# Kernel optimization log

Hardware: AMD Instinct MI355X
Metric: run time of the kernel (lower is better)

The kernel has to match this reference:

```python
import jax, jax.numpy as jnp
import numpy as np

N_NODES = 50000
N_EDGES = 800000
HEADS = 5
NFEAT = 5
C1 = 32  # hidden_layers


def setup_inputs() -> dict:
    key = jax.random.key(0)
    ks = jax.random.split(key, 20)
    s = 0.3  # glorot-ish scale
    d = {
        "x": jax.random.normal(ks[0], (N_NODES, NFEAT), jnp.float32),
        "edge_attr": jax.random.uniform(ks[1], (N_EDGES, 1), jnp.float32),
        "src": jax.random.randint(ks[2], (N_EDGES,), 0, N_NODES, jnp.int32),
        "dst": jax.random.randint(ks[3], (N_EDGES,), 0, N_NODES, jnp.int32),
        # conv1: in=5 -> heads=5, out=32, concat
        "W1": jax.random.normal(ks[4], (NFEAT, HEADS * C1), jnp.float32) * s,
        "a_src1": jax.random.normal(ks[5], (HEADS, C1), jnp.float32) * s,
        "a_dst1": jax.random.normal(ks[6], (HEADS, C1), jnp.float32) * s,
        "We1": jax.random.normal(ks[7], (1, HEADS * C1), jnp.float32) * s,
        "ae1": jax.random.normal(ks[8], (HEADS, C1), jnp.float32) * s,
        "b1": jnp.zeros((HEADS * C1,), jnp.float32),
        # conv2: in=160 -> heads=5, out=1, mean over heads
        "W2": jax.random.normal(ks[9], (HEADS * C1, HEADS * 1), jnp.float32) * 0.08,
        "a_src2": jax.random.normal(ks[10], (HEADS, 1), jnp.float32) * s,
        "a_dst2": jax.random.normal(ks[11], (HEADS, 1), jnp.float32) * s,
        "We2": jax.random.normal(ks[12], (1, HEADS * 1), jnp.float32) * s,
        "ae2": jax.random.normal(ks[13], (HEADS, 1), jnp.float32) * s,
        "b2": jnp.zeros((1,), jnp.float32),
        "Wlin": jax.random.normal(ks[14], (1, 1), jnp.float32),
    }
    return d


def gat_layer(x, src, dst, eattr, W, a_src, a_dst, We, a_e, bias, concat, n_nodes):
    """PyG GATConv with edge_dim, self-loops already added by caller."""
    H, C = a_src.shape
    h = (x @ W).reshape(-1, H, C)                      # [N,H,C]
    alpha_s = (h * a_src[None]).sum(-1)                # [N,H]
    alpha_d = (h * a_dst[None]).sum(-1)                # [N,H]
    ee = (eattr @ We).reshape(-1, H, C)                # [E,H,C]
    alpha_e = (ee * a_e[None]).sum(-1)                 # [E,H]
    logits = jax.nn.leaky_relu(alpha_s[src] + alpha_d[dst] + alpha_e, 0.2)
    # segment softmax over destination nodes
    m = jax.ops.segment_max(logits, dst, num_segments=n_nodes)
    m = jnp.where(jnp.isfinite(m), m, 0.0)
    ex = jnp.exp(logits - m[dst])
    denom = jax.ops.segment_sum(ex, dst, num_segments=n_nodes)
    alpha = ex / (denom[dst] + 1e-16)                  # [E,H]
    msg = (alpha[:, :, None] * h[src]).reshape(-1, H * C)
    agg = jax.ops.segment_sum(msg, dst, num_segments=n_nodes).reshape(n_nodes, H, C)
    if concat:
        return agg.reshape(n_nodes, H * C) + bias
    return agg.mean(axis=1) + bias


def reference(x, edge_attr, src, dst, W1, a_src1, a_dst1, We1, ae1, b1,
              W2, a_src2, a_dst2, We2, ae2, b2, Wlin):
    n = x.shape[0]
    loop = jnp.arange(n, dtype=src.dtype)
    s = jnp.concatenate([src, loop])
    t = jnp.concatenate([dst, loop])
    # self-loop edge_attr = mean of edge_attr (PyG fill_value='mean')
    ea_loop = jnp.broadcast_to(edge_attr.mean(axis=0, keepdims=True), (n, edge_attr.shape[1]))
    ea = jnp.concatenate([edge_attr, ea_loop], axis=0)

    x1 = gat_layer(x, s, t, ea, W1, a_src1, a_dst1, We1, ae1, b1, True, n)
    x2 = jax.nn.relu(x1)
    # dropout p=0.2 is identity in eval mode
    x4 = gat_layer(x2, s, t, ea, W2, a_src2, a_dst2, We2, ae2, b2, False, n)
    x5 = x4 @ Wlin                                     # Linear(1,1,bias=False)
    return jax.nn.sigmoid(x5)                          # [N,1]
```

## Files before the change

kernel.cpp:

```cpp
#include <hip/hip_runtime.h>
#include <hip/hip_fp16.h>
#include <math.h>

#define N_NODES 50000
#define N_EDGES 800000
#define E2 (N_EDGES + N_NODES)
#define HEADS 5
#define C1 32
#define F1 160

#define BSZ 64
#define NBK 782
#define NBL 128
#define CH  6641
#define MTOT (NBK*NBL)
#define MC  391
#define GRID_H1 (N_NODES/4)
#define CAP 1408

static constexpr size_t alignup(size_t x){ return (x + 255) & ~size_t(255); }
static constexpr size_t OFF_SCAL  = 0;
static constexpr size_t OFF_H     = alignup(OFF_SCAL + 64*4);
static constexpr size_t OFF_EAS   = alignup(OFF_H    + (size_t)MTOT*4);
static constexpr size_t OFF_PART  = alignup(OFF_EAS  + (size_t)NBL*4);
static constexpr size_t OFF_PPREF = alignup(OFF_PART + (size_t)MC*4);
static constexpr size_t OFF_BST   = alignup(OFF_PPREF+ (size_t)MC*4);
static constexpr size_t OFF_OFFS  = alignup(OFF_BST  + (size_t)(NBK+1)*4);
static constexpr size_t OFF_BPACK = alignup(OFF_OFFS + (size_t)(N_NODES+1)*4);
static constexpr size_t OFF_EDG   = alignup(OFF_BPACK+ (size_t)E2*8);
static constexpr size_t OFF_AS1P  = alignup(OFF_EDG  + (size_t)E2*4);
static constexpr size_t OFF_AD1P  = alignup(OFF_AS1P + (size_t)N_NODES*8*4);
static constexpr size_t OFF_IDEN1 = alignup(OFF_AD1P + (size_t)N_NODES*8*4);
static constexpr size_t OFF_G16   = alignup(OFF_IDEN1+ (size_t)N_NODES*8*4);
static constexpr size_t OFF_AD2P  = alignup(OFF_G16  + (size_t)N_NODES*16*2);
static constexpr size_t OFF_H1Q   = alignup(OFF_AD2P + (size_t)N_NODES*8*4);
static constexpr size_t OFF_X2H   = alignup(OFF_H1Q  + (size_t)N_NODES*F1);
static constexpr size_t OFF_ALPH  = alignup(OFF_X2H  + (size_t)N_NODES*F1*2);

typedef float vf2 __attribute__((ext_vector_type(2)));
__device__ __forceinline__ float2 fp8x2_to_f32(unsigned short r){
  vf2 v = __builtin_amdgcn_cvt_pk_f32_fp8((int)r, false);
  return make_float2(v.x, v.y);
}
__device__ __forceinline__ float4 fp8x4_to_f32(unsigned int r){
  vf2 lo = __builtin_amdgcn_cvt_pk_f32_fp8((int)r, false);
  vf2 hi = __builtin_amdgcn_cvt_pk_f32_fp8((int)r, true);
  return make_float4(lo.x, lo.y, hi.x, hi.y);
}

__global__ __launch_bounds__(320) void k_init(const float* __restrict__ x, const float* __restrict__ W1,
                       const float* __restrict__ as1w, const float* __restrict__ ad1w,
                       unsigned short* __restrict__ h1q, float* __restrict__ as1p, float* __restrict__ ad1p,
                       const int* __restrict__ dst, const float* __restrict__ ea,
                       int* __restrict__ H, float* __restrict__ easum){
  __shared__ float sW[5*F1];
  int t = threadIdx.x;
  if (blockIdx.x < GRID_H1){
    for (int k = t; k < 5*F1; k += 320) sW[k] = W1[k];
    __syncthreads();
    int nl = t / 80;
    int c  = t - nl*80;
    int n  = blockIdx.x*4 + nl;
    int c0 = 2*c;
    float hv0 = 0.f, hv1 = 0.f;
    #pragma unroll
    for (int f = 0; f < 5; f++){
      float xv = x[n*5 + f];
      hv0 += xv * sW[f*F1 + c0];
      hv1 += xv * sW[f*F1 + c0 + 1];
    }
    int pk = __builtin_amdgcn_cvt_pk_fp8_f32(hv0, hv1, 0, false);
    h1q[n*80 + c] = (unsigned short)(pk & 0xFFFF);
    float vs = hv0*as1w[c0] + hv1*as1w[c0+1];
    float vd = hv0*ad1w[c0] + hv1*ad1w[c0+1];
    #pragma unroll
    for (int m = 8; m >= 1; m >>= 1){
      vs += __shfl_xor(vs, m, 64);
      vd += __shfl_xor(vd, m, 64);
    }
    if ((c & 15) == 0){
      int h = c >> 4;
      as1p[n*8 + h] = vs;
      ad1p[n*8 + h] = vd;
    }
  } else {
    int* hist = (int*)sW;
    float* wsum = (float*)&hist[NBK + 1];
    for (int k = t; k < NBK; k += 320) hist[k] = 0;
    __syncthreads();
    int b = blockIdx.x - GRID_H1;
    int e0 = b*CH, e1 = min(e0 + CH, E2);
    float s = 0.f;
    for (int e = e0 + t; e < e1; e += 320){
      int d;
      if (e < N_EDGES){ d = dst[e]; s += ea[e]; }
      else d = e - N_EDGES;
      atomicAdd(&hist[d >> 6], 1);
    }
    #pragma unroll
    for (int m = 1; m < 64; m <<= 1) s += __shfl_xor(s, m, 64);
    if ((t & 63) == 0) wsum[t >> 6] = s;
    __syncthreads();
    for (int k = t; k < NBK; k += 320) H[(size_t)k*NBL + b] = hist[k];
    if (t == 0) easum[b] = wsum[0] + wsum[1] + wsum[2] + wsum[3] + wsum[4];
  }
}

__global__ void k_s1(const int* __restrict__ H, int* __restrict__ partial){
  int i = blockIdx.x*256 + threadIdx.x;
  int v = (i < MTOT) ? H[i] : 0;
  #pragma unroll
  for (int m = 1; m < 64; m <<= 1) v += __shfl_xor(v, m, 64);
  __shared__ int sh[4];
  if ((threadIdx.x & 63) == 0) sh[threadIdx.x >> 6] = v;
  __syncthreads();
  if (threadIdx.x == 0) partial[blockIdx.x] = sh[0] + sh[1] + sh[2] + sh[3];
}

__global__ __launch_bounds__(512) void k_s2p(const int* __restrict__ partial, int* __restrict__ ppref,
                      int* __restrict__ offs, int* __restrict__ bstart,
                      const float* __restrict__ easum,
                      const float* __restrict__ We1, const float* __restrict__ ae1,
                      const float* __restrict__ We2, const float* __restrict__ ae2,
                      float* __restrict__ scal){
  __shared__ int sp[512];
  __shared__ float sh_ea[NBL];
  int t = threadIdx.x;
  if (t < NBL) sh_ea[t] = easum[t];
  if (t >= 448 && t < 448 + HEADS){
    int h = t - 448;
    float s = 0.f;
    for (int c = 0; c < C1; c++) s += We1[h*C1 + c] * ae1[h*C1 + c];
    scal[2 + h] = s;
    scal[7 + h] = We2[h] * ae2[h];
  }
  int v = (t < MC) ? partial[t] : 0;
  sp[t] = v;
  __syncthreads();
  if (t == 511){
    float es = 0.f;
    for (int i = 0; i < NBL; i++) es += sh_ea[i];
    scal[1] = es / (float)N_EDGES;
  }
  for (int off = 1; off < 512; off <<= 1){
    int u = (t >= off) ? sp[t - off] : 0;
    __syncthreads();
    sp[t] += u;
    __syncthreads();
  }
  if (t < MC) ppref[t] = sp[t] - v;
  if (t == 0){ offs[N_NODES] = E2; bstart[NBK] = E2; }
}

__global__ void k_s3(int* __restrict__ H, const int* __restrict__ ppref, int* __restrict__ bstart){
  __shared__ int sp[256];
  int b = blockIdx.x, t = threadIdx.x;
  int i = b*256 + t;
  int v = (i < MTOT) ? H[i] : 0;
  sp[t] = v;
  __syncthreads();
  for (int off = 1; off < 256; off <<= 1){
    int u = (t >= off) ? sp[t - off] : 0;
    __syncthreads();
    sp[t] += u;
    __syncthreads();
  }
  int P = ppref[b] + sp[t] - v;
  if (i < MTOT){
    H[i] = P;
    if (i % NBL == 0) bstart[i / NBL] = P;
  }
}

__global__ __launch_bounds__(256) void k_scat(const int* __restrict__ src, const int* __restrict__ dst,
                       const float* __restrict__ ea, const float* __restrict__ scal,
                       const int* __restrict__ H, int2* __restrict__ bpack){
  __shared__ int lofs[NBK];
  int b = blockIdx.x;
  for (int k = threadIdx.x; k < NBK; k += 256) lofs[k] = H[(size_t)k*NBL + b];
  __syncthreads();
  float mean = scal[1];
  int e0 = b*CH, e1 = min(e0 + CH, E2);
  for (int e = e0 + threadIdx.x; e < e1; e += 256){
    int d, s; float a;
    if (e < N_EDGES){ d = dst[e]; s = src[e]; a = ea[e]; }
    else { d = s = e - N_EDGES; a = mean; }
    int pos = atomicAdd(&lofs[d >> 6], 1);
    bpack[pos] = make_int2(s | ((d & 63) << 16), __float_as_int(a));
  }
}

__global__ __launch_bounds__(256) void k_final2(const int* __restrict__ bstart,
                        const int2* __restrict__ bpack,
                        const float* __restrict__ as1p, const float* __restrict__ ad1p,
                        const float* __restrict__ scal,
                        int* __restrict__ offs, unsigned int* __restrict__ edge2,
                        __half* __restrict__ alpha, float* __restrict__ iden1){
  __shared__ int   cnt[BSZ], cur[BSZ];
  __shared__ float denL[BSZ*HEADS];
  __shared__ float adL [BSZ*HEADS];
  __shared__ unsigned int s_edge[CAP];
  __shared__ __half s_al[HEADS][CAP];
  int k = blockIdx.x, t = threadIdx.x;
  int base = k*BSZ;
  if (t < BSZ) cnt[t] = 0;
  for (int i = t; i < BSZ*HEADS; i += 256){
    int node = base + i/HEADS;
    adL[i] = (node < N_NODES) ? ad1p[node*8 + i%HEADS] : 0.f;
    denL[i] = 0.f;
  }
  __syncthreads();
  int r0 = bstart[k], r1 = bstart[k + 1];
  int sz = r1 - r0;
  for (int j = r0 + t; j < r1; j += 256) atomicAdd(&cnt[(bpack[j].x >> 16) & 63], 1);
  __syncthreads();
  if (t == 0){
    int run = 0;
    for (int i = 0; i < BSZ; i++){ int c = cnt[i]; cnt[i] = run; cur[i] = run; run += c; }
  }
  __syncthreads();
  if (t < BSZ){
    int n = base + t;
    if (n < N_NODES) offs[n] = r0 + cnt[t];
  }
  float wd[HEADS];
  #pragma unroll
  for (int h = 0; h < HEADS; h++) wd[h] = scal[2 + h];

  if (sz <= CAP){
    for (int j = r0 + t; j < r1; j += 256){
      int2 v = bpack[j];
      int s = v.x & 0xFFFF, loc = (v.x >> 16) & 63;
      float ea = __int_as_float(v.y);
      int lp = atomicAdd(&cur[loc], 1);
      s_edge[lp] = (unsigned int)s |
                   ((unsigned int)__half_as_ushort(__float2half(ea)) << 16);
      float4 g4 = *(const float4*)(as1p + s*8);
      float g5 = as1p[s*8 + 4];
      float g[HEADS] = {g4.x, g4.y, g4.z, g4.w, g5};
      #pragma unroll
      for (int h = 0; h < HEADS; h++){
        float lg = g[h] + adL[loc*HEADS + h] + ea*wd[h];
        lg = fmaxf(lg, 0.2f*lg);
        lg = fminf(lg, 10.f);
        float p = __expf(lg);
        s_al[h][lp] = __float2half(p);
        atomicAdd(&denL[loc*HEADS + h], p);
      }
    }
    __syncthreads();
    for (int i = t; i < sz; i += 256) edge2[r0 + i] = s_edge[i];
    #pragma unroll
    for (int h = 0; h < HEADS; h++)
      for (int i = t; i < sz; i += 256)
        alpha[(size_t)h*E2 + r0 + i] = s_al[h][i];
  } else {
    for (int j = r0 + t; j < r1; j += 256){
      int2 v = bpack[j];
      int s = v.x & 0xFFFF, loc = (v.x >> 16) & 63;
      float ea = __int_as_float(v.y);
      int pos = r0 + atomicAdd(&cur[loc], 1);
      edge2[pos] = (unsigned int)s |
                   ((unsigned int)__half_as_ushort(__float2half(ea)) << 16);
      float4 g4 = *(const float4*)(as1p + s*8);
      float g5 = as1p[s*8 + 4];
      float g[HEADS] = {g4.x, g4.y, g4.z, g4.w, g5};
      #pragma unroll
      for (int h = 0; h < HEADS; h++){
        float lg = g[h] + adL[loc*HEADS + h] + ea*wd[h];
        lg = fmaxf(lg, 0.2f*lg);
        lg = fminf(lg, 10.f);
        float p = __expf(lg);
        alpha[(size_t)h*E2 + pos] = __float2half(p);
        atomicAdd(&denL[loc*HEADS + h], p);
      }
    }
    __syncthreads();
  }
  for (int i = t; i < BSZ*HEADS; i += 256){
    int node = base + i/HEADS;
    if (node < N_NODES) iden1[node*8 + i%HEADS] = 1.f/(denL[i] + 1e-16f);
  }
}

__global__ __launch_bounds__(320) void k_agg1(const int* __restrict__ offs,
                      const unsigned int* __restrict__ edge2,
                      const __half* __restrict__ alpha, const float* __restrict__ iden1,
                      const unsigned short* __restrict__ h1q,
                      const float* __restrict__ b1, __half* __restrict__ x2h){
  int nl = threadIdx.x / 40;
  int c4 = threadIdx.x - nl*40;
  int n  = blockIdx.x*8 + nl;
  int h  = c4 >> 3;
  const __half* aph = alpha + (size_t)h*E2;
  const unsigned int* h1row = (const unsigned int*)h1q;
  int j0 = offs[n], j1 = offs[n + 1];
  float a0 = 0.f, a1 = 0.f, a2 = 0.f, a3 = 0.f;
  int j = j0;
  int jal = min(j1, (j0 + 3) & ~3);
  for (; j < jal; ++j){
    int s = edge2[j] & 0xFFFF;
    float a = __half2float(aph[j]);
    float4 f = fp8x4_to_f32(h1row[(size_t)s*40 + c4]);
    a0 += a*f.x; a1 += a*f.y; a2 += a*f.z; a3 += a*f.w;
  }
  for (; j + 7 < j1; j += 8){
    uint4  sa = *(const uint4*)(edge2 + j);
    uint4  sb = *(const uint4*)(edge2 + j + 4);
    union { uint2 u; __half2 h[2]; } UA; UA.u = *(const uint2*)(aph + j);
    union { uint2 u; __half2 h[2]; } UB; UB.u = *(const uint2*)(aph + j + 4);
    float2 A01 = __half22float2(UA.h[0]);
    float2 A23 = __half22float2(UA.h[1]);
    float2 A45 = __half22float2(UB.h[0]);
    float2 A67 = __half22float2(UB.h[1]);
    unsigned int r0 = h1row[(size_t)(sa.x & 0xFFFF)*40 + c4];
    unsigned int r1 = h1row[(size_t)(sa.y & 0xFFFF)*40 + c4];
    unsigned int r2 = h1row[(size_t)(sa.z & 0xFFFF)*40 + c4];
    unsigned int r3 = h1row[(size_t)(sa.w & 0xFFFF)*40 + c4];
    unsigned int r4 = h1row[(size_t)(sb.x & 0xFFFF)*40 + c4];
    unsigned int r5 = h1row[(size_t)(sb.y & 0xFFFF)*40 + c4];
    unsigned int r6 = h1row[(size_t)(sb.z & 0xFFFF)*40 + c4];
    unsigned int r7 = h1row[(size_t)(sb.w & 0xFFFF)*40 + c4];
    float4 f0 = fp8x4_to_f32(r0), f1 = fp8x4_to_f32(r1);
    float4 f2 = fp8x4_to_f32(r2), f3 = fp8x4_to_f32(r3);
    float4 f4 = fp8x4_to_f32(r4), f5 = fp8x4_to_f32(r5);
    float4 f6 = fp8x4_to_f32(r6), f7 = fp8x4_to_f32(r7);
    a0 += A01.x*f0.x; a1 += A01.x*f0.y; a2 += A01.x*f0.z; a3 += A01.x*f0.w;
    a0 += A01.y*f1.x; a1 += A01.y*f1.y; a2 += A01.y*f1.z; a3 += A01.y*f1.w;
    a0 += A23.x*f2.x; a1 += A23.x*f2.y; a2 += A23.x*f2.z; a3 += A23.x*f2.w;
    a0 += A23.y*f3.x; a1 += A23.y*f3.y; a2 += A23.y*f3.z; a3 += A23.y*f3.w;
    a0 += A45.x*f4.x; a1 += A45.x*f4.y; a2 += A45.x*f4.z; a3 += A45.x*f4.w;
    a0 += A45.y*f5.x; a1 += A45.y*f5.y; a2 += A45.y*f5.z; a3 += A45.y*f5.w;
    a0 += A67.x*f6.x; a1 += A67.x*f6.y; a2 += A67.x*f6.z; a3 += A67.x*f6.w;
    a0 += A67.y*f7.x; a1 += A67.y*f7.y; a2 += A67.y*f7.z; a3 += A67.y*f7.w;
  }
  for (; j + 3 < j1; j += 4){
    uint4  ss = *(const uint4*)(edge2 + j);
    union { uint2 u; __half2 h[2]; } UA; UA.u = *(const uint2*)(aph + j);
    float2 A01 = __half22float2(UA.h[0]);
    float2 A23 = __half22float2(UA.h[1]);
    float4 f0 = fp8x4_to_f32(h1row[(size_t)(ss.x & 0xFFFF)*40 + c4]);
    float4 f1 = fp8x4_to_f32(h1row[(size_t)(ss.y & 0xFFFF)*40 + c4]);
    float4 f2 = fp8x4_to_f32(h1row[(size_t)(ss.z & 0xFFFF)*40 + c4]);
    float4 f3 = fp8x4_to_f32(h1row[(size_t)(ss.w & 0xFFFF)*40 + c4]);
    a0 += A01.x*f0.x; a1 += A01.x*f0.y; a2 += A01.x*f0.z; a3 += A01.x*f0.w;
    a0 += A01.y*f1.x; a1 += A01.y*f1.y; a2 += A01.y*f1.z; a3 += A01.y*f1.w;
    a0 += A23.x*f2.x; a1 += A23.x*f2.y; a2 += A23.x*f2.z; a3 += A23.x*f2.w;
    a0 += A23.y*f3.x; a1 += A23.y*f3.y; a2 += A23.y*f3.z; a3 += A23.y*f3.w;
  }
  for (; j < j1; ++j){
    int s = edge2[j] & 0xFFFF;
    float a = __half2float(aph[j]);
    float4 f = fp8x4_to_f32(h1row[(size_t)s*40 + c4]);
    a0 += a*f.x; a1 += a*f.y; a2 += a*f.z; a3 += a*f.w;
  }
  float inv = iden1[n*8 + h];
  float4 bb = *(const float4*)(b1 + 4*c4);
  float v0 = fmaxf(a0*inv + bb.x, 0.f);
  float v1 = fmaxf(a1*inv + bb.y, 0.f);
  float v2 = fmaxf(a2*inv + bb.z, 0.f);
  float v3 = fmaxf(a3*inv + bb.w, 0.f);
  __half2 o0 = __floats2half2_rn(v0, v1);
  __half2 o1 = __floats2half2_rn(v2, v3);
  *(uint2*)(x2h + (size_t)n*F1 + 4*c4) =
      make_uint2(*(unsigned int*)&o0, *(unsigned int*)&o1);
}

__global__ __launch_bounds__(256) void k_h2(const __half* __restrict__ x2h, const float* __restrict__ W2,
                    const float* __restrict__ asw2, const float* __restrict__ adw2,
                    __half* __restrict__ G16, float* __restrict__ ad2p){
  __shared__ float sW[F1*HEADS];
  for (int k = threadIdx.x; k < F1*HEADS; k += 256) sW[k] = W2[k];
  __syncthreads();
  int w = threadIdx.x >> 6, l = threadIdx.x & 63;
  int n = blockIdx.x*4 + w;
  const __half2* x22 = (const __half2*)x2h;
  float acc[HEADS] = {0.f, 0.f, 0.f, 0.f, 0.f};
  for (int k2 = l; k2 < 80; k2 += 64){
    float2 f = __half22float2(x22[(size_t)n*80 + k2]);
    #pragma unroll
    for (int h = 0; h < HEADS; h++)
      acc[h] += f.x * sW[(2*k2)*HEADS + h] + f.y * sW[(2*k2+1)*HEADS + h];
  }
  #pragma unroll
  for (int m = 1; m < 64; m <<= 1){
    #pragma unroll
    for (int h = 0; h < HEADS; h++) acc[h] += __shfl_xor(acc[h], m, 64);
  }
  if (l == 0){
    #pragma unroll
    for (int h = 0; h < HEADS; h++){
      G16[(size_t)n*16 + h]     = __float2half(acc[h]);
      G16[(size_t)n*16 + 5 + h] = __float2half(acc[h] * asw2[h]);
      ad2p[n*8 + h]             = acc[h] * adw2[h];
    }
    #pragma unroll
    for (int z = 10; z < 16; z++) G16[(size_t)n*16 + z] = __float2half(0.f);
  }
}

__global__ __launch_bounds__(256) void k_agg2(const int* __restrict__ offs,
                      const unsigned int* __restrict__ edge2,
                      const __half* __restrict__ G16, const float* __restrict__ ad2p,
                      const float* __restrict__ scal,
                      const float* __restrict__ b2, const float* __restrict__ Wlin,
                      float* __restrict__ out){
  int grp = threadIdx.x >> 4;
  int l16 = threadIdx.x & 15;
  int n = blockIdx.x*16 + grp;
  float adn[HEADS], wd[HEADS];
  #pragma unroll
  for (int h = 0; h < HEADS; h++){ adn[h] = ad2p[n*8 + h]; wd[h] = scal[7 + h]; }
  int j0 = offs[n], j1 = offs[n + 1];

  float den[HEADS] = {0,0,0,0,0};
  float ac[HEADS]  = {0,0,0,0,0};
  for (int j = j0 + l16; j < j1; j += 16){
    unsigned int e = edge2[j];
    int s = e & 0xFFFF;
    float c = __half2float(__ushort_as_half((unsigned short)(e >> 16)));
    const __half* gs = G16 + (size_t)s*16;
    union { uint4 u; __half2 h[4]; } U; U.u = *(const uint4*)gs;
    union { uint2 u; __half2 h[2]; } V; V.u = *(const uint2*)(gs + 8);
    float2 p01 = __half22float2(U.h[0]);
    float2 p23 = __half22float2(U.h[1]);
    float2 p45 = __half22float2(U.h[2]);
    float2 p67 = __half22float2(U.h[3]);
    float2 p89 = __half22float2(V.h[0]);
    float hv[HEADS] = {p01.x, p01.y, p23.x, p23.y, p45.x};
    float av[HEADS] = {p45.y, p67.x, p67.y, p89.x, p89.y};
    #pragma unroll
    for (int h = 0; h < HEADS; h++){
      float lg = av[h] + adn[h] + c*wd[h];
      lg = fmaxf(lg, 0.2f*lg);
      lg = fminf(lg, 50.f);
      float p = __expf(lg);
      den[h] += p;
      ac[h]  += p * hv[h];
    }
  }
  #pragma unroll
  for (int m = 1; m < 16; m <<= 1){
    #pragma unroll
    for (int h = 0; h < HEADS; h++){
      den[h] += __shfl_xor(den[h], m, 16);
      ac[h]  += __shfl_xor(ac[h], m, 16);
    }
  }
  if (l16 == 0){
    float v = 0.f;
    #pragma unroll
    for (int h = 0; h < HEADS; h++) v += ac[h] / (den[h] + 1e-16f);
    v = v * (1.f/HEADS) + b2[0];
    v *= Wlin[0];
    out[n] = 1.f / (1.f + __expf(-v));
  }
}

extern "C" void kernel_launch(void* const* d_in, const int* in_sizes, int n_in,
                              void* d_out, int out_size, void* d_ws, size_t ws_size,
                              hipStream_t stream) {
  const float* x    = (const float*)d_in[0];
  const float* ea   = (const float*)d_in[1];
  const int*   src  = (const int*)d_in[2];
  const int*   dst  = (const int*)d_in[3];
  const float* W1   = (const float*)d_in[4];
  const float* as1w = (const float*)d_in[5];
  const float* ad1w = (const float*)d_in[6];
  const float* We1  = (const float*)d_in[7];
  const float* ae1  = (const float*)d_in[8];
  const float* b1   = (const float*)d_in[9];
  const float* W2   = (const float*)d_in[10];
  const float* as2w = (const float*)d_in[11];
  const float* ad2w = (const float*)d_in[12];
  const float* We2  = (const float*)d_in[13];
  const float* ae2  = (const float*)d_in[14];
  const float* b2   = (const float*)d_in[15];
  const float* Wlin = (const float*)d_in[16];

  char* ws = (char*)d_ws;
  float* scal   = (float*)(ws + OFF_SCAL);
  int*   H      = (int*)  (ws + OFF_H);
  float* easum  = (float*)(ws + OFF_EAS);
  int*   part   = (int*)  (ws + OFF_PART);
  int*   ppref  = (int*)  (ws + OFF_PPREF);
  int*   bstart = (int*)  (ws + OFF_BST);
  int*   offs   = (int*)  (ws + OFF_OFFS);
  int2*  bpack  = (int2*) (ws + OFF_BPACK);
  unsigned int* edge2 = (unsigned int*)(ws + OFF_EDG);
  float* as1p   = (float*)(ws + OFF_AS1P);
  float* ad1p   = (float*)(ws + OFF_AD1P);
  float* iden1  = (float*)(ws + OFF_IDEN1);
  __half* G16   = (__half*)(ws + OFF_G16);
  float* ad2p   = (float*)(ws + OFF_AD2P);
  unsigned short* h1q = (unsigned short*)(ws + OFF_H1Q);
  __half* x2h   = (__half*)(ws + OFF_X2H);
  __half* alpha = (__half*)(ws + OFF_ALPH);
  float* outp   = (float*)d_out;

  k_init   <<<GRID_H1 + NBL, 320, 0, stream>>>(x, W1, as1w, ad1w, h1q, as1p, ad1p,
                                               dst, ea, H, easum);
  k_s1     <<<MC, 256, 0, stream>>>(H, part);
  k_s2p    <<<1, 512, 0, stream>>>(part, ppref, offs, bstart, easum, We1, ae1, We2, ae2, scal);
  k_s3     <<<MC, 256, 0, stream>>>(H, ppref, bstart);
  k_scat   <<<NBL, 256, 0, stream>>>(src, dst, ea, scal, H, bpack);
  k_final2 <<<NBK, 256, 0, stream>>>(bstart, bpack, as1p, ad1p, scal, offs, edge2, alpha, iden1);

  k_agg1   <<<N_NODES/8, 320, 0, stream>>>(offs, edge2, alpha, iden1, h1q, b1, x2h);
  k_h2     <<<N_NODES/4, 256, 0, stream>>>(x2h, W2, as2w, ad2w, G16, ad2p);
  k_agg2   <<<N_NODES/16, 256, 0, stream>>>(offs, edge2, G16, ad2p, scal, b2, Wlin, outp);
}
```

Before: 248.9 us.

## Fuse layer-1 attention logits and softmax denominator into aggregation kernel

Layer-1 edge attention weights and per-node softmax denominators are no longer computed in the CSR-building kernel and stored as a half-precision alpha array plus inverse-denominator array. The aggregation kernel now computes the logits, exponentials and denominator on the fly from as1p, ad1p and the packed edge attribute. This removes about 8.5 MB of alpha writes and reads, the shared-memory atomics for the denominator, and one intermediate buffer. In exchange the exp work is repeated by each of the 8 lanes sharing a head, extra gathers of as1p are added, and the 4-wide and alignment loops are dropped.

```diff
diff --git a/kernel.cpp b/kernel.cpp
--- a/kernel.cpp
+++ b/kernel.cpp
@@ -30,18 +30,12 @@
 static constexpr size_t OFF_EDG   = alignup(OFF_BPACK+ (size_t)E2*8);
 static constexpr size_t OFF_AS1P  = alignup(OFF_EDG  + (size_t)E2*4);
 static constexpr size_t OFF_AD1P  = alignup(OFF_AS1P + (size_t)N_NODES*8*4);
-static constexpr size_t OFF_IDEN1 = alignup(OFF_AD1P + (size_t)N_NODES*8*4);
-static constexpr size_t OFF_G16   = alignup(OFF_IDEN1+ (size_t)N_NODES*8*4);
+static constexpr size_t OFF_G16   = alignup(OFF_AD1P + (size_t)N_NODES*8*4);
 static constexpr size_t OFF_AD2P  = alignup(OFF_G16  + (size_t)N_NODES*16*2);
 static constexpr size_t OFF_H1Q   = alignup(OFF_AD2P + (size_t)N_NODES*8*4);
 static constexpr size_t OFF_X2H   = alignup(OFF_H1Q  + (size_t)N_NODES*F1);
-static constexpr size_t OFF_ALPH  = alignup(OFF_X2H  + (size_t)N_NODES*F1*2);
 
 typedef float vf2 __attribute__((ext_vector_type(2)));
-__device__ __forceinline__ float2 fp8x2_to_f32(unsigned short r){
-  vf2 v = __builtin_amdgcn_cvt_pk_f32_fp8((int)r, false);
-  return make_float2(v.x, v.y);
-}
 __device__ __forceinline__ float4 fp8x4_to_f32(unsigned int r){
   vf2 lo = __builtin_amdgcn_cvt_pk_f32_fp8((int)r, false);
   vf2 hi = __builtin_amdgcn_cvt_pk_f32_fp8((int)r, true);
@@ -192,23 +186,12 @@
 
 __global__ __launch_bounds__(256) void k_final2(const int* __restrict__ bstart,
                         const int2* __restrict__ bpack,
-                        const float* __restrict__ as1p, const float* __restrict__ ad1p,
-                        const float* __restrict__ scal,
-                        int* __restrict__ offs, unsigned int* __restrict__ edge2,
-                        __half* __restrict__ alpha, float* __restrict__ iden1){
-  __shared__ int   cnt[BSZ], cur[BSZ];
-  __shared__ float denL[BSZ*HEADS];
-  __shared__ float adL [BSZ*HEADS];
+                        int* __restrict__ offs, unsigned int* __restrict__ edge2){
+  __shared__ int cnt[BSZ], cur[BSZ];
   __shared__ unsigned int s_edge[CAP];
-  __shared__ __half s_al[HEADS][CAP];
   int k = blockIdx.x, t = threadIdx.x;
   int base = k*BSZ;
   if (t < BSZ) cnt[t] = 0;
-  for (int i = t; i < BSZ*HEADS; i += 256){
-    int node = base + i/HEADS;
-    adL[i] = (node < N_NODES) ? ad1p[node*8 + i%HEADS] : 0.f;
-    denL[i] = 0.f;
-  }
   __syncthreads();
   int r0 = bstart[k], r1 = bstart[k + 1];
   int sz = r1 - r0;
@@ -223,138 +206,105 @@
     int n = base + t;
     if (n < N_NODES) offs[n] = r0 + cnt[t];
   }
-  float wd[HEADS];
-  #pragma unroll
-  for (int h = 0; h < HEADS; h++) wd[h] = scal[2 + h];
-
   if (sz <= CAP){
     for (int j = r0 + t; j < r1; j += 256){
       int2 v = bpack[j];
-      int s = v.x & 0xFFFF, loc = (v.x >> 16) & 63;
-      float ea = __int_as_float(v.y);
-      int lp = atomicAdd(&cur[loc], 1);
-      s_edge[lp] = (unsigned int)s |
-                   ((unsigned int)__half_as_ushort(__float2half(ea)) << 16);
-      float4 g4 = *(const float4*)(as1p + s*8);
-      float g5 = as1p[s*8 + 4];
-      float g[HEADS] = {g4.x, g4.y, g4.z, g4.w, g5};
-      #pragma unroll
-      for (int h = 0; h < HEADS; h++){
-        float lg = g[h] + adL[loc*HEADS + h] + ea*wd[h];
-        lg = fmaxf(lg, 0.2f*lg);
-        lg = fminf(lg, 10.f);
-        float p = __expf(lg);
-        s_al[h][lp] = __float2half(p);
-        atomicAdd(&denL[loc*HEADS + h], p);
-      }
+      int lp = atomicAdd(&cur[(v.x >> 16) & 63], 1);
+      s_edge[lp] = (unsigned int)(v.x & 0xFFFF) |
+                   ((unsigned int)__half_as_ushort(__float2half(__int_as_float(v.y))) << 16);
     }
     __syncthreads();
     for (int i = t; i < sz; i += 256) edge2[r0 + i] = s_edge[i];
-    #pragma unroll
-    for (int h = 0; h < HEADS; h++)
-      for (int i = t; i < sz; i += 256)
-        alpha[(size_t)h*E2 + r0 + i] = s_al[h][i];
   } else {
     for (int j = r0 + t; j < r1; j += 256){
       int2 v = bpack[j];
-      int s = v.x & 0xFFFF, loc = (v.x >> 16) & 63;
-      float ea = __int_as_float(v.y);
-      int pos = r0 + atomicAdd(&cur[loc], 1);
-      edge2[pos] = (unsigned int)s |
-                   ((unsigned int)__half_as_ushort(__float2half(ea)) << 16);
-      float4 g4 = *(const float4*)(as1p + s*8);
-      float g5 = as1p[s*8 + 4];
-      float g[HEADS] = {g4.x, g4.y, g4.z, g4.w, g5};
-      #pragma unroll
-      for (int h = 0; h < HEADS; h++){
-        float lg = g[h] + adL[loc*HEADS + h] + ea*wd[h];
-        lg = fmaxf(lg, 0.2f*lg);
-        lg = fminf(lg, 10.f);
-        float p = __expf(lg);
-        alpha[(size_t)h*E2 + pos] = __float2half(p);
-        atomicAdd(&denL[loc*HEADS + h], p);
-      }
-    }
-    __syncthreads();
-  }
-  for (int i = t; i < BSZ*HEADS; i += 256){
-    int node = base + i/HEADS;
-    if (node < N_NODES) iden1[node*8 + i%HEADS] = 1.f/(denL[i] + 1e-16f);
+      int pos = r0 + atomicAdd(&cur[(v.x >> 16) & 63], 1);
+      edge2[pos] = (unsigned int)(v.x & 0xFFFF) |
+                   ((unsigned int)__half_as_ushort(__float2half(__int_as_float(v.y))) << 16);
+    }
   }
 }
 
 __global__ __launch_bounds__(320) void k_agg1(const int* __restrict__ offs,
                       const unsigned int* __restrict__ edge2,
-                      const __half* __restrict__ alpha, const float* __restrict__ iden1,
+                      const float* __restrict__ as1p, const float* __restrict__ ad1p,
+                      const float* __restrict__ scal,
                       const unsigned short* __restrict__ h1q,
                       const float* __restrict__ b1, __half* __restrict__ x2h){
   int nl = threadIdx.x / 40;
   int c4 = threadIdx.x - nl*40;
   int n  = blockIdx.x*8 + nl;
   int h  = c4 >> 3;
-  const __half* aph = alpha + (size_t)h*E2;
+  float wd  = scal[2 + h];
+  float adn = ad1p[n*8 + h];
   const unsigned int* h1row = (const unsigned int*)h1q;
   int j0 = offs[n], j1 = offs[n + 1];
-  float a0 = 0.f, a1 = 0.f, a2 = 0.f, a3 = 0.f;
+  float a0 = 0.f, a1 = 0.f, a2 = 0.f, a3 = 0.f, den = 0.f;
   int j = j0;
-  int jal = min(j1, (j0 + 3) & ~3);
-  for (; j < jal; ++j){
-    int s = edge2[j] & 0xFFFF;
-    float a = __half2float(aph[j]);
-    float4 f = fp8x4_to_f32(h1row[(size_t)s*40 + c4]);
-    a0 += a*f.x; a1 += a*f.y; a2 += a*f.z; a3 += a*f.w;
-  }
   for (; j + 7 < j1; j += 8){
-    uint4  sa = *(const uint4*)(edge2 + j);
-    uint4  sb = *(const uint4*)(edge2 + j + 4);
-    union { uint2 u; __half2 h[2]; } UA; UA.u = *(const uint2*)(aph + j);
-    union { uint2 u; __half2 h[2]; } UB; UB.u = *(const uint2*)(aph + j + 4);
-    float2 A01 = __half22float2(UA.h[0]);
-    float2 A23 = __half22float2(UA.h[1]);
-    float2 A45 = __half22float2(UB.h[0]);
-    float2 A67 = __half22float2(UB.h[1]);
-    unsigned int r0 = h1row[(size_t)(sa.x & 0xFFFF)*40 + c4];
-    unsigned int r1 = h1row[(size_t)(sa.y & 0xFFFF)*40 + c4];
-    unsigned int r2 = h1row[(size_t)(sa.z & 0xFFFF)*40 + c4];
-    unsigned int r3 = h1row[(size_t)(sa.w & 0xFFFF)*40 + c4];
-    unsigned int r4 = h1row[(size_t)(sb.x & 0xFFFF)*40 + c4];
-    unsigned int r5 = h1row[(size_t)(sb.y & 0xFFFF)*40 + c4];
-    unsigned int r6 = h1row[(size_t)(sb.z & 0xFFFF)*40 + c4];
-    unsigned int r7 = h1row[(size_t)(sb.w & 0xFFFF)*40 + c4];
+    uint4 sa = *(const uint4*)(edge2 + j);
+    uint4 sb = *(const uint4*)(edge2 + j + 4);
+    unsigned int e0 = sa.x, e1 = sa.y, e2v = sa.z, e3 = sa.w;
+    unsigned int e4 = sb.x, e5 = sb.y, e6 = sb.z, e7 = sb.w;
+    int s0 = e0 & 0xFFFF, s1 = e1 & 0xFFFF, s2 = e2v & 0xFFFF, s3 = e3 & 0xFFFF;
+    int s4 = e4 & 0xFFFF, s5 = e5 & 0xFFFF, s6 = e6 & 0xFFFF, s7 = e7 & 0xFFFF;
+    unsigned int r0 = h1row[(size_t)s0*40 + c4];
+    unsigned int r1 = h1row[(size_t)s1*40 + c4];
+    unsigned int r2 = h1row[(size_t)s2*40 + c4];
+    unsigned int r3 = h1row[(size_t)s3*40 + c4];
+    unsigned int r4 = h1row[(size_t)s4*40 + c4];
+    unsigned int r5 = h1row[(size_t)s5*40 + c4];
+    unsigned int r6 = h1row[(size_t)s6*40 + c4];
+    unsigned int r7 = h1row[(size_t)s7*40 + c4];
+    float g0 = as1p[s0*8 + h], g1 = as1p[s1*8 + h];
+    float g2 = as1p[s2*8 + h], g3 = as1p[s3*8 + h];
+    float g4 = as1p[s4*8 + h], g5 = as1p[s5*8 + h];
+    float g6 = as1p[s6*8 + h], g7 = as1p[s7*8 + h];
+    float c0 = __half2float(__ushort_as_half((unsigned short)(e0 >> 16)));
+    float c1 = __half2float(__ushort_as_half((unsigned short)(e1 >> 16)));
+    float c2 = __half2float(__ushort_as_half((unsigned short)(e2v >> 16)));
+    float c3 = __half2float(__ushort_as_half((unsigned short)(e3 >> 16)));
+    float c5v = __half2float(__ushort_as_half((unsigned short)(e5 >> 16)));
+    float c4v = __half2float(__ushort_as_half((unsigned short)(e4 >> 16)));
+    float c6 = __half2float(__ushort_as_half((unsigned short)(e6 >> 16)));
+    float c7 = __half2float(__ushort_as_half((unsigned short)(e7 >> 16)));
+    float l0 = g0 + adn + c0*wd;  l0 = fminf(fmaxf(l0, 0.2f*l0), 10.f);
+    float l1 = g1 + adn + c1*wd;  l1 = fminf(fmaxf(l1, 0.2f*l1), 10.f);
+    float l2 = g2 + adn + c2*wd;  l2 = fminf(fmaxf(l2, 0.2f*l2), 10.f);
+    float l3 = g3 + adn + c3*wd;  l3 = fminf(fmaxf(l3, 0.2f*l3), 10.f);
+    float l4 = g4 + adn + c4v*wd; l4 = fminf(fmaxf(l4, 0.2f*l4), 10.f);
+    float l5 = g5 + adn + c5v*wd; l5 = fminf(fmaxf(l5, 0.2f*l5), 10.f);
+    float l6 = g6 + adn + c6*wd;  l6 = fminf(fmaxf(l6, 0.2f*l6), 10.f);
+    float l7 = g7 + adn + c7*wd;  l7 = fminf(fmaxf(l7, 0.2f*l7), 10.f);
+    float p0 = __expf(l0), p1 = __expf(l1), p2 = __expf(l2), p3 = __expf(l3);
+    float p4 = __expf(l4), p5 = __expf(l5), p6 = __expf(l6), p7 = __expf(l7);
+    den += p0 + p1 + p2 + p3 + p4 + p5 + p6 + p7;
     float4 f0 = fp8x4_to_f32(r0), f1 = fp8x4_to_f32(r1);
     float4 f2 = fp8x4_to_f32(r2), f3 = fp8x4_to_f32(r3);
     float4 f4 = fp8x4_to_f32(r4), f5 = fp8x4_to_f32(r5);
     float4 f6 = fp8x4_to_f32(r6), f7 = fp8x4_to_f32(r7);
-    a0 += A01.x*f0.x; a1 += A01.x*f0.y; a2 += A01.x*f0.z; a3 += A01.x*f0.w;
-    a0 += A01.y*f1.x; a1 += A01.y*f1.y; a2 += A01.y*f1.z; a3 += A01.y*f1.w;
-    a0 += A23.x*f2.x; a1 += A23.x*f2.y; a2 += A23.x*f2.z; a3 += A23.x*f2.w;
-    a0 += A23.y*f3.x; a1 += A23.y*f3.y; a2 += A23.y*f3.z; a3 += A23.y*f3.w;
-    a0 += A45.x*f4.x; a1 += A45.x*f4.y; a2 += A45.x*f4.z; a3 += A45.x*f4.w;
-    a0 += A45.y*f5.x; a1 += A45.y*f5.y; a2 += A45.y*f5.z; a3 += A45.y*f5.w;
-    a0 += A67.x*f6.x; a1 += A67.x*f6.y; a2 += A67.x*f6.z; a3 += A67.x*f6.w;
-    a0 += A67.y*f7.x; a1 += A67.y*f7.y; a2 += A67.y*f7.z; a3 += A67.y*f7.w;
-  }
-  for (; j + 3 < j1; j += 4){
-    uint4  ss = *(const uint4*)(edge2 + j);
-    union { uint2 u; __half2 h[2]; } UA; UA.u = *(const uint2*)(aph + j);
-    float2 A01 = __half22float2(UA.h[0]);
-    float2 A23 = __half22float2(UA.h[1]);
-    float4 f0 = fp8x4_to_f32(h1row[(size_t)(ss.x & 0xFFFF)*40 + c4]);
-    float4 f1 = fp8x4_to_f32(h1row[(size_t)(ss.y & 0xFFFF)*40 + c4]);
-    float4 f2 = fp8x4_to_f32(h1row[(size_t)(ss.z & 0xFFFF)*40 + c4]);
-    float4 f3 = fp8x4_to_f32(h1row[(size_t)(ss.w & 0xFFFF)*40 + c4]);
-    a0 += A01.x*f0.x; a1 += A01.x*f0.y; a2 += A01.x*f0.z; a3 += A01.x*f0.w;
-    a0 += A01.y*f1.x; a1 += A01.y*f1.y; a2 += A01.y*f1.z; a3 += A01.y*f1.w;
-    a0 += A23.x*f2.x; a1 += A23.x*f2.y; a2 += A23.x*f2.z; a3 += A23.x*f2.w;
-    a0 += A23.y*f3.x; a1 += A23.y*f3.y; a2 += A23.y*f3.z; a3 += A23.y*f3.w;
+    a0 += p0*f0.x; a1 += p0*f0.y; a2 += p0*f0.z; a3 += p0*f0.w;
+    a0 += p1*f1.x; a1 += p1*f1.y; a2 += p1*f1.z; a3 += p1*f1.w;
+    a0 += p2*f2.x; a1 += p2*f2.y; a2 += p2*f2.z; a3 += p2*f2.w;
+    a0 += p3*f3.x; a1 += p3*f3.y; a2 += p3*f3.z; a3 += p3*f3.w;
+    a0 += p4*f4.x; a1 += p4*f4.y; a2 += p4*f4.z; a3 += p4*f4.w;
+    a0 += p5*f5.x; a1 += p5*f5.y; a2 += p5*f5.z; a3 += p5*f5.w;
+    a0 += p6*f6.x; a1 += p6*f6.y; a2 += p6*f6.z; a3 += p6*f6.w;
+    a0 += p7*f7.x; a1 += p7*f7.y; a2 += p7*f7.z; a3 += p7*f7.w;
   }
   for (; j < j1; ++j){
-    int s = edge2[j] & 0xFFFF;
-    float a = __half2float(aph[j]);
+    unsigned int e = edge2[j];
+    int s = e & 0xFFFF;
+    float c = __half2float(__ushort_as_half((unsigned short)(e >> 16)));
+    float g = as1p[s*8 + h];
+    float lg = g + adn + c*wd;
+    lg = fminf(fmaxf(lg, 0.2f*lg), 10.f);
+    float p = __expf(lg);
+    den += p;
     float4 f = fp8x4_to_f32(h1row[(size_t)s*40 + c4]);
-    a0 += a*f.x; a1 += a*f.y; a2 += a*f.z; a3 += a*f.w;
-  }
-  float inv = iden1[n*8 + h];
+    a0 += p*f.x; a1 += p*f.y; a2 += p*f.z; a3 += p*f.w;
+  }
+  float inv = 1.f / (den + 1e-16f);
   float4 bb = *(const float4*)(b1 + 4*c4);
   float v0 = fmaxf(a0*inv + bb.x, 0.f);
   float v1 = fmaxf(a1*inv + bb.y, 0.f);
@@ -490,12 +440,10 @@
   unsigned int* edge2 = (unsigned int*)(ws + OFF_EDG);
   float* as1p   = (float*)(ws + OFF_AS1P);
   float* ad1p   = (float*)(ws + OFF_AD1P);
-  float* iden1  = (float*)(ws + OFF_IDEN1);
   __half* G16   = (__half*)(ws + OFF_G16);
   float* ad2p   = (float*)(ws + OFF_AD2P);
   unsigned short* h1q = (unsigned short*)(ws + OFF_H1Q);
   __half* x2h   = (__half*)(ws + OFF_X2H);
-  __half* alpha = (__half*)(ws + OFF_ALPH);
   float* outp   = (float*)d_out;
 
   k_init   <<<GRID_H1 + NBL, 320, 0, stream>>>(x, W1, as1w, ad1w, h1q, as1p, ad1p,
@@ -504,9 +452,9 @@
   k_s2p    <<<1, 512, 0, stream>>>(part, ppref, offs, bstart, easum, We1, ae1, We2, ae2, scal);
   k_s3     <<<MC, 256, 0, stream>>>(H, ppref, bstart);
   k_scat   <<<NBL, 256, 0, stream>>>(src, dst, ea, scal, H, bpack);
-  k_final2 <<<NBK, 256, 0, stream>>>(bstart, bpack, as1p, ad1p, scal, offs, edge2, alpha, iden1);
-
-  k_agg1   <<<N_NODES/8, 320, 0, stream>>>(offs, edge2, alpha, iden1, h1q, b1, x2h);
+  k_final2 <<<NBK, 256, 0, stream>>>(bstart, bpack, offs, edge2);
+
+  k_agg1   <<<N_NODES/8, 320, 0, stream>>>(offs, edge2, as1p, ad1p, scal, h1q, b1, x2h);
   k_h2     <<<N_NODES/4, 256, 0, stream>>>(x2h, W2, as2w, ad2w, G16, ad2p);
   k_agg2   <<<N_NODES/16, 256, 0, stream>>>(offs, edge2, G16, ad2p, scal, b2, Wlin, outp);
 }
```

New measurement: 225.6 us. -9.4%, faster.
